# Optimization experiments

Measured on AMD Instinct MI355X. Metric: run time of the kernel, lower is better.

Reference implementation:

```python
import jax, jax.numpy as jnp
import numpy as np

B, N, D, H = 8, 577, 768, 12
HD = D // H
SCALE = HD ** -0.5
LN_EPS = 1e-5


def layer_norm(x, w, b):
    mu = jnp.mean(x, -1, keepdims=True)
    var = jnp.mean((x - mu) ** 2, -1, keepdims=True)
    return (x - mu) * jax.lax.rsqrt(var + LN_EPS) * w + b


def wasserstein_distance_matmul(mean1, cov1, mean2, cov2):
    # all [B,H,N,hd]; returns [B,H,N,N]
    m1_2 = jnp.sum(mean1 ** 2, -1, keepdims=True)
    m2_2 = jnp.sum(mean2 ** 2, -1, keepdims=True)
    ret = -2.0 * jnp.einsum('bhnd,bhmd->bhnm', mean1, mean2) + m1_2 + jnp.swapaxes(m2_2, -1, -2)
    c1s = jnp.sqrt(jnp.clip(cov1, 1e-24))
    c2s = jnp.sqrt(jnp.clip(cov2, 1e-24))
    cov_ret = (-2.0 * jnp.einsum('bhnd,bhmd->bhnm', c1s, c2s)
               + jnp.sum(cov1, -1, keepdims=True)
               + jnp.swapaxes(jnp.sum(cov2, -1, keepdims=True), -1, -2))
    return ret + cov_ret


def setup_inputs() -> dict:
    key = jax.random.key(0)
    ks = jax.random.split(key, 20)
    s = 0.02
    return {
        'x_mean': jax.random.normal(ks[0], (B, N, D), jnp.float32),
        'x_cov': jax.random.normal(ks[1], (B, N, D), jnp.float32),
        'rel_pos_bias': jax.random.normal(ks[2], (1, H, N, N), jnp.float32),
        'norm1_w': jnp.ones((D,), jnp.float32),
        'norm1_b': jnp.zeros((D,), jnp.float32),
        'qkv_w': jax.random.normal(ks[3], (3 * D, D), jnp.float32) * s,
        'proj_w': jax.random.normal(ks[4], (D, D), jnp.float32) * s,
        'proj_b': jnp.zeros((D,), jnp.float32),
        'cov_proj_w': jax.random.normal(ks[5], (D, D), jnp.float32) * s,
        'cov_proj_b': jnp.zeros((D,), jnp.float32),
        'norm2_w': jnp.ones((D,), jnp.float32),
        'norm2_b': jnp.zeros((D,), jnp.float32),
        'fc1_w': jax.random.normal(ks[6], (4 * D, D), jnp.float32) * s,
        'fc1_b': jnp.zeros((4 * D,), jnp.float32),
        'fc2_w': jax.random.normal(ks[7], (D, 4 * D), jnp.float32) * s,
        'fc2_b': jnp.zeros((D,), jnp.float32),
        'gamma1': 0.1 * jnp.ones((D,), jnp.float32),
        'gamma2': 0.1 * jnp.ones((D,), jnp.float32),
    }


def _split_heads(t):
    # [B,N,3D] -> q,k,v each [B,H,N,hd]
    t = t.reshape(B, N, 3, H, HD).transpose(2, 0, 3, 1, 4)
    return t[0], t[1], t[2]


def attention(xm, xc, rel_pos_bias, qkv_w, proj_w, proj_b, cov_proj_w, cov_proj_b):
    qkv = xm @ qkv_w.T                                  # [B,N,3D]
    q, k, v = _split_heads(qkv)
    cov_qkv = jax.nn.elu(xc @ qkv_w.T) + 1.0            # same weights for cov stream
    cov_q, cov_k, cov_v = _split_heads(cov_qkv)
    q = q * SCALE
    attn = -wasserstein_distance_matmul(q, cov_q, k, cov_k)
    attn = jax.nn.sigmoid(attn + 1e-24)
    attn = jax.nn.softmax(attn + rel_pos_bias, axis=-1)  # [B,H,N,N]
    mean_ctx = jnp.einsum('bhnm,bhmd->bhnd', attn, v).transpose(0, 2, 1, 3).reshape(B, N, D)
    cov_ctx = jnp.einsum('bhnm,bhmd->bhnd', attn ** 2, cov_v).transpose(0, 2, 1, 3).reshape(B, N, D)
    mean_out = mean_ctx @ proj_w.T + proj_b
    cov_out = cov_ctx @ cov_proj_w.T + cov_proj_b
    return mean_out, cov_out


def mlp(x, fc1_w, fc1_b, fc2_w, fc2_b):
    h = jax.nn.gelu(x @ fc1_w.T + fc1_b, approximate=False)
    return h @ fc2_w.T + fc2_b


def reference(x_mean, x_cov, rel_pos_bias, norm1_w, norm1_b, qkv_w, proj_w, proj_b,
              cov_proj_w, cov_proj_b, norm2_w, norm2_b, fc1_w, fc1_b, fc2_w, fc2_b,
              gamma1, gamma2):
    mean, cov = attention(layer_norm(x_mean, norm1_w, norm1_b),
                          layer_norm(x_cov, norm1_w, norm1_b),
                          rel_pos_bias, qkv_w, proj_w, proj_b, cov_proj_w, cov_proj_b)
    x_mean = x_mean + gamma1 * mean
    fcm = gamma2 * mlp(layer_norm(x_mean, norm2_w, norm2_b), fc1_w, fc1_b, fc2_w, fc2_b)
    x_cov = x_cov + gamma1 * cov
    fcc = gamma2 * mlp(layer_norm(x_cov, norm2_w, norm2_b), fc1_w, fc1_b, fc2_w, fc2_b)
    return (x_mean + fcm, x_cov + fcc)
```

## Files before the change

### kernel.cpp

```cpp
#include <hip/hip_runtime.h>
#include <hip/hip_bf16.h>
#include <math.h>
#include <stdint.h>

typedef __bf16 bf16;
typedef __attribute__((ext_vector_type(8))) __bf16 bf16x8;
typedef __attribute__((ext_vector_type(4))) float f32x4;

typedef __attribute__((address_space(1))) void gas_void;
typedef __attribute__((address_space(3))) void las_void;

#define DEV __device__ __forceinline__

static constexpr int B_ = 8, N_ = 577, D_ = 768, H_ = 12;
static constexpr int M_ = B_ * N_;
static constexpr int MP_ = 4736;
static constexpr int NP_ = 640;
static constexpr int BH_ = B_ * H_;
static constexpr float SCALE_ = 0.125f;

DEV void async_cp16(const void* g, void* l) {
  __builtin_amdgcn_global_load_lds((gas_void*)g, (las_void*)l, 16, 0, 0);
}
DEV float fast_rcp(float x) { return __builtin_amdgcn_rcpf(x); }
DEV float elu1(float x) { return x > 0.0f ? x + 1.0f : __expf(x); }
DEV float fast_gelu(float x) {
  const float x2 = x * x;
  const float z = x * fmaf(0.0713548826f, x2, 1.5957691216f);
  return x * fast_rcp(1.0f + __expf(-z));
}

__global__ __launch_bounds__(256) void cvt_kernel(const float* __restrict__ src,
                                                  bf16* __restrict__ dst, int n4) {
  const int i = blockIdx.x * 256 + threadIdx.x;
  if (i < n4) {
    const float4 v = ((const float4*)src)[i];
    bf16 o[4] = {(bf16)v.x, (bf16)v.y, (bf16)v.z, (bf16)v.w};
    *(uint64_t*)(dst + (size_t)i * 4) = *(const uint64_t*)o;
  }
}

__global__ __launch_bounds__(256) void ln_kernel(const float* __restrict__ x,
                                                 const float* __restrict__ w,
                                                 const float* __restrict__ bp,
                                                 bf16* __restrict__ out) {
  const int row = blockIdx.x;
  const int t = threadIdx.x;
  const float* xr = x + (size_t)row * D_;
  float v0 = xr[t], v1 = xr[t + 256], v2 = xr[t + 512];
  float s = v0 + v1 + v2;
  float ss = v0 * v0 + v1 * v1 + v2 * v2;
#pragma unroll
  for (int m = 32; m >= 1; m >>= 1) {
    s += __shfl_down(s, m);
    ss += __shfl_down(ss, m);
  }
  __shared__ float red[8];
  if ((t & 63) == 0) { red[t >> 6] = s; red[4 + (t >> 6)] = ss; }
  __syncthreads();
  s = red[0] + red[1] + red[2] + red[3];
  ss = red[4] + red[5] + red[6] + red[7];
  const float mu = s * (1.0f / D_);
  float var = ss * (1.0f / D_) - mu * mu;
  var = fmaxf(var, 0.0f);
  const float rs = rsqrtf(var + 1e-5f);
  bf16* orow = out + (size_t)row * D_;
  orow[t]       = (bf16)((v0 - mu) * rs * w[t]       + bp[t]);
  orow[t + 256] = (bf16)((v1 - mu) * rs * w[t + 256] + bp[t + 256]);
  orow[t + 512] = (bf16)((v2 - mu) * rs * w[t + 512] + bp[t + 512]);
}

enum { EP_BF16 = 0, EP_PROJ = 1, EP_GELU = 2, EP_FC2 = 3 };

template <int EP, int K>
__global__ __launch_bounds__(256) void gemm_bt(
    const bf16* __restrict__ A, const bf16* __restrict__ W0,
    const bf16* __restrict__ W1, int Nn, int gx,
    const float* __restrict__ bias0, const float* __restrict__ bias1,
    const float* __restrict__ gamma,
    const float* __restrict__ resid0, const float* __restrict__ resid1,
    bf16* __restrict__ Cb, float* __restrict__ Cf0, float* __restrict__ Cf1) {
  __shared__ __align__(16) bf16 As[3][128 * 32];
  __shared__ __align__(16) bf16 Bs[3][128 * 32];
  const int nwg = gridDim.x;
  const int o = blockIdx.x;
  const int q = nwg >> 3, r = nwg & 7, xcd = o & 7;
  const int flat = (xcd < r ? xcd * (q + 1) : r * (q + 1) + (xcd - r) * q) + (o >> 3);
  const int bx = flat % gx, by = flat / gx;

  const int t = threadIdx.x;
  const int lane = t & 63, wv = t >> 6;
  const int ln = lane & 15, kg = lane >> 4;
  const int wr = wv >> 1, wc = wv & 1;
  const int s = (int)(by >= (MP_ / 128));
  const bf16* W = s ? W1 : W0;
  const size_t brow = (size_t)by * 128;
  const size_t bcol = (size_t)bx * 128;
  const int r0 = t >> 2, gsl = t & 3;
  const bf16* A0 = A + (brow + r0) * (size_t)K + gsl * 8;
  const bf16* A1 = A + (brow + r0 + 64) * (size_t)K + gsl * 8;
  const bf16* W0p = W + (bcol + r0) * (size_t)K + gsl * 8;
  const bf16* W1p = W + (bcol + r0 + 64) * (size_t)K + gsl * 8;

  auto stage = [&](int buf, int kk) {
    async_cp16(A0 + kk, &As[buf][(wv * 64) * 8]);
    async_cp16(A1 + kk, &As[buf][(256 + wv * 64) * 8]);
    async_cp16(W0p + kk, &Bs[buf][(wv * 64) * 8]);
    async_cp16(W1p + kk, &Bs[buf][(256 + wv * 64) * 8]);
  };

  f32x4 acc[4][4] = {};
  constexpr int nt = K >> 5;
  static_assert(nt % 3 == 0, "K/32 must be divisible by 3");
  stage(0, 0);
  stage(1, 32);
#pragma unroll 1
  for (int tb = 0; tb < nt; tb += 3) {
#pragma unroll
    for (int u = 0; u < 3; u++) {
      const int tt = tb + u;
      if (tt + 1 < nt) {
        asm volatile("s_waitcnt vmcnt(4)" ::: "memory");
      } else {
        asm volatile("s_waitcnt vmcnt(0)" ::: "memory");
      }
      __builtin_amdgcn_s_barrier();
      bf16x8 af[4], bfr[4];
#pragma unroll
      for (int i = 0; i < 4; i++)
        af[i] = *(const bf16x8*)&As[u][(wr * 64 + i * 16 + ln) * 32 + kg * 8];
#pragma unroll
      for (int j = 0; j < 4; j++)
        bfr[j] = *(const bf16x8*)&Bs[u][(wc * 64 + j * 16 + ln) * 32 + kg * 8];
#pragma unroll
      for (int i = 0; i < 4; i++)
#pragma unroll
        for (int j = 0; j < 4; j++)
          acc[i][j] = __builtin_amdgcn_mfma_f32_16x16x32_bf16(af[i], bfr[j], acc[i][j], 0, 0, 0);
      if (tt + 2 < nt) stage((u + 2) % 3, (tt + 2) * 32);
    }
  }

  const float* biasS = s ? bias1 : bias0;
  const float* residS = s ? resid1 : resid0;
  float* CfS = s ? Cf1 : Cf0;
#pragma unroll
  for (int i = 0; i < 4; i++) {
    const int rb = (int)brow + wr * 64 + i * 16 + kg * 4;
#pragma unroll
    for (int j = 0; j < 4; j++) {
      const int col = (int)bcol + wc * 64 + j * 16 + ln;
#pragma unroll
      for (int rr = 0; rr < 4; rr++) {
        const int row = rb + rr;
        float v = acc[i][j][rr];
        if (EP == EP_BF16) {
          Cb[(size_t)row * Nn + col] = (bf16)v;
        } else if (EP == EP_GELU) {
          v += biasS[col];
          Cb[(size_t)row * Nn + col] = (bf16)fast_gelu(v);
        } else {
          const int r2 = row - s * MP_;
          if (r2 < M_) {
            v += biasS[col];
            if (EP == EP_PROJ) {
              CfS[(size_t)r2 * Nn + col] = residS[(size_t)r2 * Nn + col] + gamma[col] * v;
            } else {
              CfS[(size_t)r2 * Nn + col] += gamma[col] * v;
            }
          }
        }
      }
    }
  }
}

__global__ __launch_bounds__(256) void prep_kernel(
    const bf16* __restrict__ qm, const bf16* __restrict__ qc,
    bf16* __restrict__ Qcat, bf16* __restrict__ Kcat,
    bf16* __restrict__ Vt, bf16* __restrict__ CVt,
    float* __restrict__ rowt, float* __restrict__ colt) {
  const int n0 = blockIdx.x * 64;
  const int h = blockIdx.y, b = blockIdx.z;
  const int bh = b * H_ + h;
  const int t = threadIdx.x;
  const int nl = t >> 2, c = t & 3;
  const int n = n0 + nl;
  const bool valid = n < N_;
  __shared__ bf16 vts[64][72], cvts[64][72];
  float q2 = 0.f, cqs = 0.f, k2 = 0.f, cks = 0.f;
  bf16 qo[16], sqo[16], ko[16], sko[16];
  if (valid) {
    const size_t ro = (size_t)(b * N_ + n) * 2304 + h * 64 + c * 16;
#pragma unroll
    for (int half = 0; half < 2; half++) {
      bf16x8 qv8 = *(const bf16x8*)(qm + ro + half * 8);
      bf16x8 kv8 = *(const bf16x8*)(qm + ro + 768 + half * 8);
      bf16x8 vv8 = *(const bf16x8*)(qm + ro + 1536 + half * 8);
      bf16x8 cq8 = *(const bf16x8*)(qc + ro + half * 8);
      bf16x8 ck8 = *(const bf16x8*)(qc + ro + 768 + half * 8);
      bf16x8 cv8 = *(const bf16x8*)(qc + ro + 1536 + half * 8);
#pragma unroll
      for (int i = 0; i < 8; i++) {
        const int d = half * 8 + i;
        float qv = (float)qv8[i] * SCALE_;
        float kv = (float)kv8[i];
        float cq1 = elu1((float)cq8[i]);
        float ck1 = elu1((float)ck8[i]);
        q2 += qv * qv; cqs += cq1; k2 += kv * kv; cks += ck1;
        qo[d] = (bf16)qv; sqo[d] = (bf16)sqrtf(fmaxf(cq1, 1e-24f));
        ko[d] = (bf16)kv; sko[d] = (bf16)sqrtf(fmaxf(ck1, 1e-24f));
        vts[nl][c * 16 + d] = vv8[i];
        cvts[nl][c * 16 + d] = (bf16)elu1((float)cv8[i]);
      }
    }
  } else {
#pragma unroll
    for (int d = 0; d < 16; d++) {
      qo[d] = (bf16)0.f; sqo[d] = (bf16)0.f; ko[d] = (bf16)0.f; sko[d] = (bf16)0.f;
      vts[nl][c * 16 + d] = (bf16)0.f; cvts[nl][c * 16 + d] = (bf16)0.f;
    }
  }
  {
    bf16* qrow = Qcat + ((size_t)bh * NP_ + n) * 128;
    bf16* krow = Kcat + ((size_t)bh * NP_ + n) * 128;
#pragma unroll
    for (int d = 0; d < 16; d++) {
      qrow[c * 16 + d] = qo[d];
      qrow[64 + c * 16 + d] = sqo[d];
      krow[c * 16 + d] = ko[d];
      krow[64 + c * 16 + d] = sko[d];
    }
  }
  float rt = q2 + cqs, ct = k2 + cks;
  rt += __shfl_xor(rt, 1); rt += __shfl_xor(rt, 2);
  ct += __shfl_xor(ct, 1); ct += __shfl_xor(ct, 2);
  if (c == 0) { rowt[(size_t)bh * NP_ + n] = rt; colt[(size_t)bh * NP_ + n] = ct; }
  __syncthreads();
  const int drow = t >> 2;
  const size_t vb = ((size_t)bh * 64 + drow) * NP_ + n0 + c * 16;
#pragma unroll
  for (int i = 0; i < 16; i++) {
    Vt[vb + i] = vts[c * 16 + i][drow];
    CVt[vb + i] = cvts[c * 16 + i][drow];
  }
}

__global__ __launch_bounds__(256) void attn_kernel(
    const bf16* __restrict__ Qcat, const bf16* __restrict__ Kcat,
    const bf16* __restrict__ Vt, const bf16* __restrict__ CVt,
    const float* __restrict__ rowt, const float* __restrict__ colt,
    const bf16* __restrict__ bias,
    bf16* __restrict__ ctxm, bf16* __restrict__ ctxc) {
  const int id = blockIdx.x;
  const int xcd = id & 7, slot = id >> 3;
  const int g = xcd + 8 * (slot / 10);
  const int it = slot % 10;
  const int b = g / H_, h = g % H_;
  const int bh = g;
  const int i0 = it * 64;
  const int t = threadIdx.x;
  const int lane = t & 63, w = t >> 6;
  const int ln = lane & 15, kg = lane >> 4;
  __shared__ __align__(16) bf16 Ks[64 * 128];
  __shared__ __align__(16) bf16 Vs[64 * 64];
  __shared__ __align__(16) bf16 CVs[64 * 64];
  __shared__ __align__(16) bf16 Ps[64 * 72];

  const bf16* Qg = Qcat + (size_t)bh * NP_ * 128;
  const bf16* Kg = Kcat + (size_t)bh * NP_ * 128;
  const bf16* Vg = Vt + (size_t)bh * 64 * NP_;
  const bf16* CVg = CVt + (size_t)bh * 64 * NP_;

#pragma unroll
  for (int qq = 0; qq < 4; qq++) {
    const int idx = qq * 256 + t;
    const int row = idx >> 4, sl = idx & 15;
    async_cp16(Qg + (size_t)(i0 + row) * 128 + ((sl ^ (row & 7)) * 8),
               &Ks[(qq * 256 + w * 64) * 8]);
  }
  __syncthreads();
  bf16x8 aq[4];
  {
    const int row = w * 16 + ln;
#pragma unroll
    for (int kc = 0; kc < 4; kc++) {
      const int slot2 = kc * 4 + kg;
      aq[kc] = *(const bf16x8*)&Ks[row * 128 + ((slot2 ^ (row & 7)) * 8)];
    }
  }
  float rt[4];
#pragma unroll
  for (int r = 0; r < 4; r++) rt[r] = rowt[(size_t)bh * NP_ + i0 + w * 16 + kg * 4 + r];

  f32x4 accm[4] = {}, accc[4] = {};
  float den[4] = {0.f, 0.f, 0.f, 0.f};
  const int igb = i0 + w * 16 + kg * 4;

  for (int jt = 0; jt < 10; jt++) {
    const int j0 = jt * 64;
    __syncthreads();
#pragma unroll
    for (int qq = 0; qq < 4; qq++) {
      const int idx = qq * 256 + t;
      const int row = idx >> 4, sl = idx & 15;
      async_cp16(Kg + (size_t)(j0 + row) * 128 + ((sl ^ (row & 7)) * 8),
                 &Ks[(qq * 256 + w * 64) * 8]);
    }
#pragma unroll
    for (int qq = 0; qq < 2; qq++) {
      const int idx = qq * 256 + t;
      const int row = idx >> 3, sl = idx & 7;
      async_cp16(Vg + (size_t)row * NP_ + j0 + ((sl ^ (row & 7)) * 8),
                 &Vs[(qq * 256 + w * 64) * 8]);
      async_cp16(CVg + (size_t)row * NP_ + j0 + ((sl ^ (row & 7)) * 8),
                 &CVs[(qq * 256 + w * 64) * 8]);
    }
    float bb[4][4], ctb[4];
#pragma unroll
    for (int js = 0; js < 4; js++) {
      const int jg = j0 + js * 16 + ln;
      const int jc = jg < N_ ? jg : N_ - 1;
      ctb[js] = colt[(size_t)bh * NP_ + jg];
#pragma unroll
      for (int r = 0; r < 4; r++) {
        const int ic = (igb + r) < N_ ? (igb + r) : N_ - 1;
        bb[js][r] = (float)bias[((size_t)h * N_ + ic) * N_ + jc];
      }
    }
    __syncthreads();
#pragma unroll
    for (int js = 0; js < 4; js++) {
      f32x4 sv = {};
#pragma unroll
      for (int kc = 0; kc < 4; kc++) {
        const int row = js * 16 + ln;
        const int slot2 = kc * 4 + kg;
        bf16x8 bk = *(const bf16x8*)&Ks[row * 128 + ((slot2 ^ (row & 7)) * 8)];
        sv = __builtin_amdgcn_mfma_f32_16x16x32_bf16(aq[kc], bk, sv, 0, 0, 0);
      }
      const int jg = j0 + js * 16 + ln;
#pragma unroll
      for (int r = 0; r < 4; r++) {
        const float S = 2.0f * sv[r] - rt[r] - ctb[js];
        const float sig = fast_rcp(1.0f + __expf(-S));
        float e = __expf(sig + bb[js][r]);
        if (jg >= N_) e = 0.0f;
        const bf16 eb = (bf16)e;
        den[r] += (float)eb;
        Ps[(w * 16 + kg * 4 + r) * 72 + js * 16 + ln] = eb;
      }
    }
#pragma unroll
    for (int ks = 0; ks < 2; ks++) {
      const int prow = w * 16 + ln;
      bf16x8 pa = *(const bf16x8*)&Ps[prow * 72 + ks * 32 + kg * 8];
      bf16x8 p2a;
#pragma unroll
      for (int i = 0; i < 8; i++) {
        const float pf = (float)pa[i];
        p2a[i] = (bf16)(pf * pf);
      }
#pragma unroll
      for (int nt = 0; nt < 4; nt++) {
        const int vrow = nt * 16 + ln;
        const int slot2 = ks * 4 + kg;
        bf16x8 vb = *(const bf16x8*)&Vs[vrow * 64 + ((slot2 ^ (vrow & 7)) * 8)];
        bf16x8 cvb = *(const bf16x8*)&CVs[vrow * 64 + ((slot2 ^ (vrow & 7)) * 8)];
        accm[nt] = __builtin_amdgcn_mfma_f32_16x16x32_bf16(pa, vb, accm[nt], 0, 0, 0);
        accc[nt] = __builtin_amdgcn_mfma_f32_16x16x32_bf16(p2a, cvb, accc[nt], 0, 0, 0);
      }
    }
  }
#pragma unroll
  for (int r = 0; r < 4; r++) {
    float d = den[r];
    d += __shfl_xor(d, 1); d += __shfl_xor(d, 2);
    d += __shfl_xor(d, 4); d += __shfl_xor(d, 8);
    den[r] = d;
  }
#pragma unroll
  for (int r = 0; r < 4; r++) {
    const int ig = i0 + w * 16 + kg * 4 + r;
    if (ig < N_) {
      const float inv = fast_rcp(den[r]);
      const float inv2 = inv * inv;
      const size_t base = (size_t)(b * N_ + ig) * D_ + h * 64;
#pragma unroll
      for (int nt = 0; nt < 4; nt++) {
        ctxm[base + nt * 16 + ln] = (bf16)(accm[nt][r] * inv);
        ctxc[base + nt * 16 + ln] = (bf16)(accc[nt][r] * inv2);
      }
    }
  }
}

extern "C" void kernel_launch(void* const* d_in, const int* in_sizes, int n_in,
                              void* d_out, int out_size, void* d_ws, size_t ws_size,
                              hipStream_t stream) {
  const float* x_mean = (const float*)d_in[0];
  const float* x_cov  = (const float*)d_in[1];
  const float* rpb    = (const float*)d_in[2];
  const float* n1w    = (const float*)d_in[3];
  const float* n1b    = (const float*)d_in[4];
  const float* qkvw   = (const float*)d_in[5];
  const float* projw  = (const float*)d_in[6];
  const float* projb  = (const float*)d_in[7];
  const float* cprojw = (const float*)d_in[8];
  const float* cprojb = (const float*)d_in[9];
  const float* n2w    = (const float*)d_in[10];
  const float* n2b    = (const float*)d_in[11];
  const float* fc1w   = (const float*)d_in[12];
  const float* fc1b   = (const float*)d_in[13];
  const float* fc2w   = (const float*)d_in[14];
  const float* fc2b   = (const float*)d_in[15];
  const float* g1     = (const float*)d_in[16];
  const float* g2     = (const float*)d_in[17];
  (void)in_sizes; (void)n_in; (void)out_size; (void)ws_size;

  char* ws = (char*)d_ws;
  size_t off = 0;
  auto take = [&](size_t bytes) {
    char* p = ws + off;
    off += (bytes + 255) & ~(size_t)255;
    return p;
  };
  bf16* wq   = (bf16*)take((size_t)2304 * 768 * 2);
  bf16* wp   = (bf16*)take((size_t)768 * 768 * 2);
  bf16* wcp  = (bf16*)take((size_t)768 * 768 * 2);
  bf16* wf1  = (bf16*)take((size_t)3072 * 768 * 2);
  bf16* wf2  = (bf16*)take((size_t)768 * 3072 * 2);
  bf16* xln  = (bf16*)take((size_t)2 * MP_ * 768 * 2);
  char* R    = take((size_t)2 * MP_ * 3072 * 2);
  bf16* qkvb = (bf16*)R;
  bf16* hbuf = (bf16*)R;
  bf16* biasb = (bf16*)(R + (size_t)2 * MP_ * 2304 * 2);
  bf16* Qcat = (bf16*)take((size_t)BH_ * NP_ * 128 * 2);
  bf16* Kcat = (bf16*)take((size_t)BH_ * NP_ * 128 * 2);
  bf16* Vt   = (bf16*)take((size_t)BH_ * 64 * NP_ * 2);
  bf16* CVt  = (bf16*)take((size_t)BH_ * 64 * NP_ * 2);
  float* rowt = (float*)take((size_t)BH_ * NP_ * 4);
  float* colt = (float*)take((size_t)BH_ * NP_ * 4);
  bf16* ctx  = (bf16*)take((size_t)2 * MP_ * 768 * 2);

  float* outm = (float*)d_out;
  float* outc = outm + (size_t)M_ * D_;

  cvt_kernel<<<(2304 * 768 / 4 + 255) / 256, 256, 0, stream>>>(qkvw, wq, 2304 * 768 / 4);
  cvt_kernel<<<(768 * 768 / 4 + 255) / 256, 256, 0, stream>>>(projw, wp, 768 * 768 / 4);
  cvt_kernel<<<(768 * 768 / 4 + 255) / 256, 256, 0, stream>>>(cprojw, wcp, 768 * 768 / 4);
  cvt_kernel<<<(3072 * 768 / 4 + 255) / 256, 256, 0, stream>>>(fc1w, wf1, 3072 * 768 / 4);
  cvt_kernel<<<(768 * 3072 / 4 + 255) / 256, 256, 0, stream>>>(fc2w, wf2, 768 * 3072 / 4);
  cvt_kernel<<<(H_ * N_ * N_ / 4 + 255) / 256, 256, 0, stream>>>(rpb, biasb, H_ * N_ * N_ / 4);
  ln_kernel<<<M_, 256, 0, stream>>>(x_mean, n1w, n1b, xln);
  ln_kernel<<<M_, 256, 0, stream>>>(x_cov, n1w, n1b, xln + (size_t)MP_ * 768);
  gemm_bt<EP_BF16, 768><<<18 * 74, 256, 0, stream>>>(xln, wq, wq, 2304, 18,
      nullptr, nullptr, nullptr, nullptr, nullptr, qkvb, nullptr, nullptr);
  prep_kernel<<<dim3(10, 12, 8), 256, 0, stream>>>(
      qkvb, qkvb + (size_t)MP_ * 2304, Qcat, Kcat, Vt, CVt, rowt, colt);
  attn_kernel<<<960, 256, 0, stream>>>(Qcat, Kcat, Vt, CVt, rowt, colt, biasb,
                                       ctx, ctx + (size_t)MP_ * 768);
  gemm_bt<EP_PROJ, 768><<<6 * 74, 256, 0, stream>>>(ctx, wp, wcp, 768, 6,
      projb, cprojb, g1, x_mean, x_cov, nullptr, outm, outc);
  ln_kernel<<<M_, 256, 0, stream>>>(outm, n2w, n2b, xln);
  ln_kernel<<<M_, 256, 0, stream>>>(outc, n2w, n2b, xln + (size_t)MP_ * 768);
  gemm_bt<EP_GELU, 768><<<24 * 74, 256, 0, stream>>>(xln, wf1, wf1, 3072, 24,
      fc1b, fc1b, nullptr, nullptr, nullptr, hbuf, nullptr, nullptr);
  gemm_bt<EP_FC2, 3072><<<6 * 74, 256, 0, stream>>>(hbuf, wf2, wf2, 768, 6,
      fc2b, fc2b, g2, nullptr, nullptr, nullptr, outm, outc);
}
```

Measured before the change: 385.7 us.

## Enlarge GEMM tiles to 256x128 with 8 waves and earlier prefetch issue

The GEMM kernel moves from a 128x128 tile with 4 waves to a 256x128 tile with 8 waves (512 threads), so each staged weight tile is reused across twice as many rows. A rows are clamped and stores are masked so tiles can straddle the padded boundary between the mean and cov halves. The prefetch of the next stage is also issued right after the barrier instead of after the MFMAs, for better overlap of loads with compute. The risks are fewer workgroups, which hurts wave fill for the smaller proj and fc2 GEMMs, plus wasted work in the padded rows of the last tile.

```diff
diff --git a/kernel.cpp b/kernel.cpp
--- a/kernel.cpp
+++ b/kernel.cpp
@@ -73,40 +73,45 @@
 enum { EP_BF16 = 0, EP_PROJ = 1, EP_GELU = 2, EP_FC2 = 3 };
 
 template <int EP, int K>
-__global__ __launch_bounds__(256) void gemm_bt(
-    const bf16* __restrict__ A, const bf16* __restrict__ W0,
-    const bf16* __restrict__ W1, int Nn, int gx,
+__global__ __launch_bounds__(512, 4) void gemm_bt(
+    const bf16* __restrict__ A0, const bf16* __restrict__ A1,
+    const bf16* __restrict__ W0, const bf16* __restrict__ W1,
+    int Nn, int gx,
     const float* __restrict__ bias0, const float* __restrict__ bias1,
     const float* __restrict__ gamma,
     const float* __restrict__ resid0, const float* __restrict__ resid1,
     bf16* __restrict__ Cb, float* __restrict__ Cf0, float* __restrict__ Cf1) {
-  __shared__ __align__(16) bf16 As[3][128 * 32];
-  __shared__ __align__(16) bf16 Bs[3][128 * 32];
+  __shared__ __align__(16) bf16 As[3 * 8192];
+  __shared__ __align__(16) bf16 Bs[3 * 4096];
   const int nwg = gridDim.x;
   const int o = blockIdx.x;
   const int q = nwg >> 3, r = nwg & 7, xcd = o & 7;
   const int flat = (xcd < r ? xcd * (q + 1) : r * (q + 1) + (xcd - r) * q) + (o >> 3);
   const int bx = flat % gx, by = flat / gx;
 
+  const int s = (int)(by >= 19);
+  const int byl = by - (s ? 19 : 0);
+  const bf16* A = s ? A1 : A0;
+  const bf16* W = s ? W1 : W0;
+  const int brow = byl * 256;
+  const int bcol = bx * 128;
+
   const int t = threadIdx.x;
   const int lane = t & 63, wv = t >> 6;
   const int ln = lane & 15, kg = lane >> 4;
   const int wr = wv >> 1, wc = wv & 1;
-  const int s = (int)(by >= (MP_ / 128));
-  const bf16* W = s ? W1 : W0;
-  const size_t brow = (size_t)by * 128;
-  const size_t bcol = (size_t)bx * 128;
+
   const int r0 = t >> 2, gsl = t & 3;
-  const bf16* A0 = A + (brow + r0) * (size_t)K + gsl * 8;
-  const bf16* A1 = A + (brow + r0 + 64) * (size_t)K + gsl * 8;
-  const bf16* W0p = W + (bcol + r0) * (size_t)K + gsl * 8;
-  const bf16* W1p = W + (bcol + r0 + 64) * (size_t)K + gsl * 8;
+  const int ra0 = min(brow + r0, MP_ - 1);
+  const int ra1 = min(brow + 128 + r0, MP_ - 1);
+  const bf16* Asrc0 = A + (size_t)ra0 * K + gsl * 8;
+  const bf16* Asrc1 = A + (size_t)ra1 * K + gsl * 8;
+  const bf16* Bsrc  = W + (size_t)(bcol + r0) * K + gsl * 8;
 
   auto stage = [&](int buf, int kk) {
-    async_cp16(A0 + kk, &As[buf][(wv * 64) * 8]);
-    async_cp16(A1 + kk, &As[buf][(256 + wv * 64) * 8]);
-    async_cp16(W0p + kk, &Bs[buf][(wv * 64) * 8]);
-    async_cp16(W1p + kk, &Bs[buf][(256 + wv * 64) * 8]);
+    async_cp16(Asrc0 + kk, &As[buf * 8192 + wv * 512]);
+    async_cp16(Asrc1 + kk, &As[buf * 8192 + 4096 + wv * 512]);
+    async_cp16(Bsrc + kk,  &Bs[buf * 4096 + wv * 512]);
   };
 
   f32x4 acc[4][4] = {};
@@ -114,30 +119,33 @@
   static_assert(nt % 3 == 0, "K/32 must be divisible by 3");
   stage(0, 0);
   stage(1, 32);
+  const int aoff = (wr * 64 + ln) * 32 + kg * 8;
+  const int boff = (wc * 64 + ln) * 32 + kg * 8;
 #pragma unroll 1
   for (int tb = 0; tb < nt; tb += 3) {
 #pragma unroll
     for (int u = 0; u < 3; u++) {
       const int tt = tb + u;
       if (tt + 1 < nt) {
-        asm volatile("s_waitcnt vmcnt(4)" ::: "memory");
+        asm volatile("s_waitcnt vmcnt(3)" ::: "memory");
       } else {
         asm volatile("s_waitcnt vmcnt(0)" ::: "memory");
       }
       __builtin_amdgcn_s_barrier();
+      asm volatile("" ::: "memory");
+      if (tt + 2 < nt) stage((u + 2) % 3, (tt + 2) * 32);
       bf16x8 af[4], bfr[4];
 #pragma unroll
       for (int i = 0; i < 4; i++)
-        af[i] = *(const bf16x8*)&As[u][(wr * 64 + i * 16 + ln) * 32 + kg * 8];
+        af[i] = *(const bf16x8*)&As[u * 8192 + aoff + i * 512];
 #pragma unroll
       for (int j = 0; j < 4; j++)
-        bfr[j] = *(const bf16x8*)&Bs[u][(wc * 64 + j * 16 + ln) * 32 + kg * 8];
+        bfr[j] = *(const bf16x8*)&Bs[u * 4096 + boff + j * 512];
 #pragma unroll
       for (int i = 0; i < 4; i++)
 #pragma unroll
         for (int j = 0; j < 4; j++)
           acc[i][j] = __builtin_amdgcn_mfma_f32_16x16x32_bf16(af[i], bfr[j], acc[i][j], 0, 0, 0);
-      if (tt + 2 < nt) stage((u + 2) % 3, (tt + 2) * 32);
     }
   }
 
@@ -146,28 +154,30 @@
   float* CfS = s ? Cf1 : Cf0;
 #pragma unroll
   for (int i = 0; i < 4; i++) {
-    const int rb = (int)brow + wr * 64 + i * 16 + kg * 4;
+    const int rb = brow + wr * 64 + i * 16 + kg * 4;
 #pragma unroll
     for (int j = 0; j < 4; j++) {
-      const int col = (int)bcol + wc * 64 + j * 16 + ln;
+      const int col = bcol + wc * 64 + j * 16 + ln;
 #pragma unroll
       for (int rr = 0; rr < 4; rr++) {
-        const int row = rb + rr;
+        const int rowl = rb + rr;
         float v = acc[i][j][rr];
         if (EP == EP_BF16) {
-          Cb[(size_t)row * Nn + col] = (bf16)v;
+          if (rowl < MP_) Cb[((size_t)(s * MP_ + rowl)) * Nn + col] = (bf16)v;
         } else if (EP == EP_GELU) {
-          v += biasS[col];
-          Cb[(size_t)row * Nn + col] = (bf16)fast_gelu(v);
+          if (rowl < MP_) {
+            v += biasS[col];
+            Cb[((size_t)(s * MP_ + rowl)) * Nn + col] = (bf16)fast_gelu(v);
+          }
+        } else if (EP == EP_PROJ) {
+          if (rowl < M_) {
+            v += biasS[col];
+            CfS[(size_t)rowl * Nn + col] = residS[(size_t)rowl * Nn + col] + gamma[col] * v;
+          }
         } else {
-          const int r2 = row - s * MP_;
-          if (r2 < M_) {
+          if (rowl < M_) {
             v += biasS[col];
-            if (EP == EP_PROJ) {
-              CfS[(size_t)r2 * Nn + col] = residS[(size_t)r2 * Nn + col] + gamma[col] * v;
-            } else {
-              CfS[(size_t)r2 * Nn + col] += gamma[col] * v;
-            }
+            CfS[(size_t)rowl * Nn + col] += gamma[col] * v;
           }
         }
       }
@@ -454,18 +464,22 @@
   cvt_kernel<<<(H_ * N_ * N_ / 4 + 255) / 256, 256, 0, stream>>>(rpb, biasb, H_ * N_ * N_ / 4);
   ln_kernel<<<M_, 256, 0, stream>>>(x_mean, n1w, n1b, xln);
   ln_kernel<<<M_, 256, 0, stream>>>(x_cov, n1w, n1b, xln + (size_t)MP_ * 768);
-  gemm_bt<EP_BF16, 768><<<18 * 74, 256, 0, stream>>>(xln, wq, wq, 2304, 18,
+  gemm_bt<EP_BF16, 768><<<18 * 38, 512, 0, stream>>>(
+      xln, xln + (size_t)MP_ * 768, wq, wq, 2304, 18,
       nullptr, nullptr, nullptr, nullptr, nullptr, qkvb, nullptr, nullptr);
   prep_kernel<<<dim3(10, 12, 8), 256, 0, stream>>>(
       qkvb, qkvb + (size_t)MP_ * 2304, Qcat, Kcat, Vt, CVt, rowt, colt);
   attn_kernel<<<960, 256, 0, stream>>>(Qcat, Kcat, Vt, CVt, rowt, colt, biasb,
                                        ctx, ctx + (size_t)MP_ * 768);
-  gemm_bt<EP_PROJ, 768><<<6 * 74, 256, 0, stream>>>(ctx, wp, wcp, 768, 6,
+  gemm_bt<EP_PROJ, 768><<<6 * 38, 512, 0, stream>>>(
+      ctx, ctx + (size_t)MP_ * 768, wp, wcp, 768, 6,
       projb, cprojb, g1, x_mean, x_cov, nullptr, outm, outc);
   ln_kernel<<<M_, 256, 0, stream>>>(outm, n2w, n2b, xln);
   ln_kernel<<<M_, 256, 0, stream>>>(outc, n2w, n2b, xln + (size_t)MP_ * 768);
-  gemm_bt<EP_GELU, 768><<<24 * 74, 256, 0, stream>>>(xln, wf1, wf1, 3072, 24,
+  gemm_bt<EP_GELU, 768><<<24 * 38, 512, 0, stream>>>(
+      xln, xln + (size_t)MP_ * 768, wf1, wf1, 3072, 24,
       fc1b, fc1b, nullptr, nullptr, nullptr, hbuf, nullptr, nullptr);
-  gemm_bt<EP_FC2, 3072><<<6 * 74, 256, 0, stream>>>(hbuf, wf2, wf2, 768, 6,
+  gemm_bt<EP_FC2, 3072><<<6 * 38, 512, 0, stream>>>(
+      hbuf, hbuf + (size_t)MP_ * 3072, wf2, wf2, 768, 6,
       fc2b, fc2b, g2, nullptr, nullptr, nullptr, outm, outc);
 }
```

Measured after the change: 403.0 us. 4.5% more time.

## Add 256x256-tile 8-wave GEMM for QKV and FC1 projections

Applied to the files above, without the earlier changes.

Introduces a new GEMM kernel with 256x256 output tiles, 512 threads and 64-wide K steps. It uses double-buffered async global-to-LDS copies with XOR-swizzled LDS layout, staggered prefetch interleaved with MFMA phases, and setprio around the MFMA bursts. The QKV and FC1 GEMMs switch to it to raise arithmetic intensity and cut LDS/global traffic per flop. The larger tile wastes more work on the padded M edge, uses 128KB of LDS, and gives fewer workgroups per GEMM, which may hurt occupancy or load balance.

```diff
diff --git a/kernel.cpp b/kernel.cpp
--- a/kernel.cpp
+++ b/kernel.cpp
@@ -72,8 +72,174 @@
 
 enum { EP_BF16 = 0, EP_PROJ = 1, EP_GELU = 2, EP_FC2 = 3 };
 
+#define MFMA16(Q)                                                                        \
+  __builtin_amdgcn_s_setprio(1);                                                         \
+  _Pragma("unroll") for (int n = 0; n < 4; ++n) {                                        \
+    acc[2*(Q)][n]   = __builtin_amdgcn_mfma_f32_16x16x32_bf16(a0, bfr[n][0], acc[2*(Q)][n], 0, 0, 0);   \
+    acc[2*(Q)][n]   = __builtin_amdgcn_mfma_f32_16x16x32_bf16(a1, bfr[n][1], acc[2*(Q)][n], 0, 0, 0);   \
+    acc[2*(Q)+1][n] = __builtin_amdgcn_mfma_f32_16x16x32_bf16(a2, bfr[n][0], acc[2*(Q)+1][n], 0, 0, 0); \
+    acc[2*(Q)+1][n] = __builtin_amdgcn_mfma_f32_16x16x32_bf16(a3, bfr[n][1], acc[2*(Q)+1][n], 0, 0, 0); \
+  }                                                                                      \
+  __builtin_amdgcn_s_setprio(0);
+
+#define LDA4(Q)                                                   \
+  bf16x8 a0, a1, a2, a3;                                          \
+  {                                                               \
+    const int rA0_ = bb + (arow + (2*(Q)) * 16) * 64;             \
+    const int rA1_ = bb + (arow + (2*(Q)+1) * 16) * 64;           \
+    a0 = *(const bf16x8*)&As[rA0_ + sw0];                         \
+    a1 = *(const bf16x8*)&As[rA0_ + sw1];                         \
+    a2 = *(const bf16x8*)&As[rA1_ + sw0];                         \
+    a3 = *(const bf16x8*)&As[rA1_ + sw1];                         \
+  }
+
+#define SYNC_PRE()                    \
+  __builtin_amdgcn_sched_barrier(0);  \
+  __builtin_amdgcn_s_barrier();       \
+  __builtin_amdgcn_sched_barrier(0);
+
+#define SYNC_POST()                   \
+  __builtin_amdgcn_sched_barrier(0);  \
+  __builtin_amdgcn_s_barrier();       \
+  __builtin_amdgcn_sched_barrier(0);
+
 template <int EP, int K>
-__global__ __launch_bounds__(256) void gemm_bt(
+__global__ __launch_bounds__(512, 2) void gemm_big(
+    const bf16* __restrict__ A0s, const bf16* __restrict__ A1s,
+    const bf16* __restrict__ W0, const bf16* __restrict__ W1,
+    int Nn, int gx, const float* __restrict__ bias,
+    bf16* __restrict__ Cb) {
+  __shared__ __align__(16) bf16 As[2 * 16384];
+  __shared__ __align__(16) bf16 Bs[2 * 16384];
+  const int nwg = gridDim.x, o = blockIdx.x;
+  const int qd = nwg >> 3, rm = nwg & 7, xcd = o & 7;
+  const int flat = (xcd < rm ? xcd * (qd + 1) : rm * (qd + 1) + (xcd - rm) * qd) + (o >> 3);
+  const int bx = flat % gx, by = flat / gx;
+  const int s = (int)(by >= 19);
+  const int brow = (by - (s ? 19 : 0)) * 256;
+  const int bcol = bx * 256;
+  const bf16* A = s ? A1s : A0s;
+  const bf16* W = s ? W1 : W0;
+
+  const int t = threadIdx.x;
+  const int w = t >> 6, l = t & 63;
+  const int ln = l & 15, kg = l >> 4;
+  const int wr = w >> 2, wc = w & 3;
+
+  const int lr = l >> 3;
+  const int lcol = ((l & 7) ^ lr) * 8;
+  const int rb0 = w * 8 + lr;
+  const int rb1 = 64 + w * 8 + lr;
+  int rA;
+  rA = brow + rb0;       rA = rA < MP_ ? rA : MP_ - 1;
+  const bf16* sA00 = A + (size_t)rA * K + lcol;
+  rA = brow + rb1;       rA = rA < MP_ ? rA : MP_ - 1;
+  const bf16* sA01 = A + (size_t)rA * K + lcol;
+  rA = brow + 128 + rb0; rA = rA < MP_ ? rA : MP_ - 1;
+  const bf16* sA10 = A + (size_t)rA * K + lcol;
+  rA = brow + 128 + rb1; rA = rA < MP_ ? rA : MP_ - 1;
+  const bf16* sA11 = A + (size_t)rA * K + lcol;
+  const bf16* sB00 = W + (size_t)(bcol + rb0) * K + lcol;
+  const bf16* sB01 = W + (size_t)(bcol + rb1) * K + lcol;
+  const bf16* sB10 = W + (size_t)(bcol + 128 + rb0) * K + lcol;
+  const bf16* sB11 = W + (size_t)(bcol + 128 + rb1) * K + lcol;
+
+  auto st2 = [&](bf16* lds0, const bf16* g0, const bf16* g1, int kk) {
+    async_cp16(g0 + kk, lds0);
+    async_cp16(g1 + kk, lds0 + 4096);
+  };
+
+  const int arow = wr * 128 + ln;
+  const int bcolr = wc * 64 + ln;
+  const int sw0 = ((0 + kg) ^ (ln & 7)) * 8;
+  const int sw1 = ((4 + kg) ^ (ln & 7)) * 8;
+
+  f32x4 acc[8][4] = {};
+  bf16x8 bfr[4][2];
+  constexpr int nkt = K / 64;
+  static_assert(K % 64 == 0, "K multiple of 64");
+
+  st2(&As[w * 512], sA00, sA01, 0);
+  st2(&As[8192 + w * 512], sA10, sA11, 0);
+  st2(&Bs[w * 512], sB00, sB01, 0);
+  st2(&Bs[8192 + w * 512], sB10, sB11, 0);
+  st2(&Bs[16384 + w * 512], sB00, sB01, 64);
+  st2(&Bs[16384 + 8192 + w * 512], sB10, sB11, 64);
+  __builtin_amdgcn_sched_barrier(0);
+  asm volatile("s_waitcnt vmcnt(4)" ::: "memory");
+  __builtin_amdgcn_s_barrier();
+  __builtin_amdgcn_sched_barrier(0);
+
+#pragma unroll 1
+  for (int tt = 0; tt < nkt; ++tt) {
+    const int bb = (tt & 1) * 16384;
+    const int bn = bb ^ 16384;
+    const int kk1 = (tt + 1) * 64, kk2 = (tt + 2) * 64;
+    const bool s1 = (tt + 1) < nkt, s2 = (tt + 2) < nkt;
+    {
+      LDA4(0)
+#pragma unroll
+      for (int n = 0; n < 4; ++n) {
+        const int cb = bb + (bcolr + n * 16) * 64;
+        bfr[n][0] = *(const bf16x8*)&Bs[cb + sw0];
+        bfr[n][1] = *(const bf16x8*)&Bs[cb + sw1];
+      }
+      if (s1) st2(&As[bn + w * 512], sA00, sA01, kk1);
+      SYNC_PRE()
+      MFMA16(0)
+      SYNC_POST()
+    }
+    {
+      LDA4(1)
+      if (s1) st2(&As[bn + 8192 + w * 512], sA10, sA11, kk1);
+      SYNC_PRE()
+      MFMA16(1)
+      SYNC_POST()
+    }
+    {
+      LDA4(2)
+      if (s2) st2(&Bs[bb + w * 512], sB00, sB01, kk2);
+      SYNC_PRE()
+      MFMA16(2)
+      SYNC_POST()
+    }
+    {
+      LDA4(3)
+      if (s2) st2(&Bs[bb + 8192 + w * 512], sB10, sB11, kk2);
+      __builtin_amdgcn_sched_barrier(0);
+      if (s2) {
+        asm volatile("s_waitcnt vmcnt(4)" ::: "memory");
+      } else if (s1) {
+        asm volatile("s_waitcnt vmcnt(0)" ::: "memory");
+      }
+      __builtin_amdgcn_s_barrier();
+      __builtin_amdgcn_sched_barrier(0);
+      MFMA16(3)
+      SYNC_POST()
+    }
+  }
+
+#pragma unroll
+  for (int m = 0; m < 8; ++m) {
+    const int rbse = brow + wr * 128 + m * 16 + kg * 4;
+#pragma unroll
+    for (int n = 0; n < 4; ++n) {
+      const int col = bcol + wc * 64 + n * 16 + ln;
+#pragma unroll
+      for (int e = 0; e < 4; ++e) {
+        const int rl = rbse + e;
+        if (rl < MP_) {
+          float v = acc[m][n][e];
+          if (EP == EP_GELU) { v += bias[col]; v = fast_gelu(v); }
+          Cb[((size_t)(s * MP_ + rl)) * Nn + col] = (bf16)v;
+        }
+      }
+    }
+  }
+}
+
+template <int EP, int K>
+__global__ __launch_bounds__(256) void gemm_sm(
     const bf16* __restrict__ A, const bf16* __restrict__ W0,
     const bf16* __restrict__ W1, int Nn, int gx,
     const float* __restrict__ bias0, const float* __restrict__ bias1,
@@ -454,18 +620,18 @@
   cvt_kernel<<<(H_ * N_ * N_ / 4 + 255) / 256, 256, 0, stream>>>(rpb, biasb, H_ * N_ * N_ / 4);
   ln_kernel<<<M_, 256, 0, stream>>>(x_mean, n1w, n1b, xln);
   ln_kernel<<<M_, 256, 0, stream>>>(x_cov, n1w, n1b, xln + (size_t)MP_ * 768);
-  gemm_bt<EP_BF16, 768><<<18 * 74, 256, 0, stream>>>(xln, wq, wq, 2304, 18,
-      nullptr, nullptr, nullptr, nullptr, nullptr, qkvb, nullptr, nullptr);
+  gemm_big<EP_BF16, 768><<<9 * 38, 512, 0, stream>>>(
+      xln, xln + (size_t)MP_ * 768, wq, wq, 2304, 9, nullptr, qkvb);
   prep_kernel<<<dim3(10, 12, 8), 256, 0, stream>>>(
       qkvb, qkvb + (size_t)MP_ * 2304, Qcat, Kcat, Vt, CVt, rowt, colt);
   attn_kernel<<<960, 256, 0, stream>>>(Qcat, Kcat, Vt, CVt, rowt, colt, biasb,
                                        ctx, ctx + (size_t)MP_ * 768);
-  gemm_bt<EP_PROJ, 768><<<6 * 74, 256, 0, stream>>>(ctx, wp, wcp, 768, 6,
+  gemm_sm<EP_PROJ, 768><<<6 * 74, 256, 0, stream>>>(ctx, wp, wcp, 768, 6,
       projb, cprojb, g1, x_mean, x_cov, nullptr, outm, outc);
   ln_kernel<<<M_, 256, 0, stream>>>(outm, n2w, n2b, xln);
   ln_kernel<<<M_, 256, 0, stream>>>(outc, n2w, n2b, xln + (size_t)MP_ * 768);
-  gemm_bt<EP_GELU, 768><<<24 * 74, 256, 0, stream>>>(xln, wf1, wf1, 3072, 24,
-      fc1b, fc1b, nullptr, nullptr, nullptr, hbuf, nullptr, nullptr);
-  gemm_bt<EP_FC2, 3072><<<6 * 74, 256, 0, stream>>>(hbuf, wf2, wf2, 768, 6,
+  gemm_big<EP_GELU, 768><<<12 * 38, 512, 0, stream>>>(
+      xln, xln + (size_t)MP_ * 768, wf1, wf1, 3072, 12, fc1b, hbuf);
+  gemm_sm<EP_FC2, 3072><<<6 * 74, 256, 0, stream>>>(hbuf, wf2, wf2, 768, 6,
       fc2b, fc2b, g2, nullptr, nullptr, nullptr, outm, outc);
 }
```

Result: slower. 412.2 us (+6.9%).

## Double-buffer K tiles in attention, load V directly to registers, merge small launches

Applied to the files above, without the earlier changes.

The attention kernel now double-buffers the K tile in shared memory, prefetching the next tile while the current one is computed. It also loads V and CV fragments straight from global memory into registers instead of staging them through LDS, which leaves one barrier per iteration instead of two. Separately, the six weight/bias conversion launches are merged into one segmented kernel, and each pair of LayerNorm launches into one. The trade-off is more register pressure from holding V fragments and uncoalesced direct global reads of V, in exchange for less launch overhead and fewer synchronisations.

```diff
diff --git a/kernel.cpp b/kernel.cpp
--- a/kernel.cpp
+++ b/kernel.cpp
@@ -30,23 +30,41 @@
   return x * fast_rcp(1.0f + __expf(-z));
 }
 
-__global__ __launch_bounds__(256) void cvt_kernel(const float* __restrict__ src,
-                                                  bf16* __restrict__ dst, int n4) {
-  const int i = blockIdx.x * 256 + threadIdx.x;
-  if (i < n4) {
-    const float4 v = ((const float4*)src)[i];
+__global__ __launch_bounds__(256) void cvt6_kernel(
+    const float* __restrict__ s0, const float* __restrict__ s1,
+    const float* __restrict__ s2, const float* __restrict__ s3,
+    const float* __restrict__ s4, const float* __restrict__ s5,
+    bf16* __restrict__ d0, bf16* __restrict__ d1, bf16* __restrict__ d2,
+    bf16* __restrict__ d3, bf16* __restrict__ d4, bf16* __restrict__ d5,
+    int n0, int n1, int n2, int n3, int n4c, int n5) {
+  const float* ss[6] = {s0, s1, s2, s3, s4, s5};
+  bf16* dd[6] = {d0, d1, d2, d3, d4, d5};
+  const int nn[6] = {n0, n1, n2, n3, n4c, n5};
+  int bid = blockIdx.x;
+  int seg = 0;
+#pragma unroll 6
+  for (int k = 0; k < 6; k++) {
+    const int nb = (nn[k] + 255) >> 8;
+    if (bid < nb) { seg = k; break; }
+    bid -= nb;
+  }
+  const int i = bid * 256 + threadIdx.x;
+  if (i < nn[seg]) {
+    const float4 v = ((const float4*)ss[seg])[i];
     bf16 o[4] = {(bf16)v.x, (bf16)v.y, (bf16)v.z, (bf16)v.w};
-    *(uint64_t*)(dst + (size_t)i * 4) = *(const uint64_t*)o;
-  }
-}
-
-__global__ __launch_bounds__(256) void ln_kernel(const float* __restrict__ x,
-                                                 const float* __restrict__ w,
-                                                 const float* __restrict__ bp,
-                                                 bf16* __restrict__ out) {
+    *(uint64_t*)(dd[seg] + (size_t)i * 4) = *(const uint64_t*)o;
+  }
+}
+
+__global__ __launch_bounds__(256) void ln2_kernel(
+    const float* __restrict__ x0, const float* __restrict__ x1,
+    const float* __restrict__ w, const float* __restrict__ bp,
+    bf16* __restrict__ out) {
   const int row = blockIdx.x;
+  const int st = (int)(row >= M_);
+  const int srow = row - st * M_;
+  const float* xr = (st ? x1 : x0) + (size_t)srow * D_;
   const int t = threadIdx.x;
-  const float* xr = x + (size_t)row * D_;
   float v0 = xr[t], v1 = xr[t + 256], v2 = xr[t + 512];
   float s = v0 + v1 + v2;
   float ss = v0 * v0 + v1 * v1 + v2 * v2;
@@ -64,7 +82,7 @@
   float var = ss * (1.0f / D_) - mu * mu;
   var = fmaxf(var, 0.0f);
   const float rs = rsqrtf(var + 1e-5f);
-  bf16* orow = out + (size_t)row * D_;
+  bf16* orow = out + ((size_t)st * MP_ + srow) * D_;
   orow[t]       = (bf16)((v0 - mu) * rs * w[t]       + bp[t]);
   orow[t + 256] = (bf16)((v1 - mu) * rs * w[t + 256] + bp[t + 256]);
   orow[t + 512] = (bf16)((v2 - mu) * rs * w[t + 512] + bp[t + 512]);
@@ -262,9 +280,7 @@
   const int t = threadIdx.x;
   const int lane = t & 63, w = t >> 6;
   const int ln = lane & 15, kg = lane >> 4;
-  __shared__ __align__(16) bf16 Ks[64 * 128];
-  __shared__ __align__(16) bf16 Vs[64 * 64];
-  __shared__ __align__(16) bf16 CVs[64 * 64];
+  __shared__ __align__(16) bf16 Ks[2][64 * 128];
   __shared__ __align__(16) bf16 Ps[64 * 72];
 
   const bf16* Qg = Qcat + (size_t)bh * NP_ * 128;
@@ -277,7 +293,14 @@
     const int idx = qq * 256 + t;
     const int row = idx >> 4, sl = idx & 15;
     async_cp16(Qg + (size_t)(i0 + row) * 128 + ((sl ^ (row & 7)) * 8),
-               &Ks[(qq * 256 + w * 64) * 8]);
+               &Ks[0][(qq * 256 + w * 64) * 8]);
+  }
+#pragma unroll
+  for (int qq = 0; qq < 4; qq++) {
+    const int idx = qq * 256 + t;
+    const int row = idx >> 4, sl = idx & 15;
+    async_cp16(Kg + (size_t)row * 128 + ((sl ^ (row & 7)) * 8),
+               &Ks[1][(qq * 256 + w * 64) * 8]);
   }
   __syncthreads();
   bf16x8 aq[4];
@@ -286,12 +309,13 @@
 #pragma unroll
     for (int kc = 0; kc < 4; kc++) {
       const int slot2 = kc * 4 + kg;
-      aq[kc] = *(const bf16x8*)&Ks[row * 128 + ((slot2 ^ (row & 7)) * 8)];
+      aq[kc] = *(const bf16x8*)&Ks[0][row * 128 + ((slot2 ^ (row & 7)) * 8)];
     }
   }
   float rt[4];
 #pragma unroll
   for (int r = 0; r < 4; r++) rt[r] = rowt[(size_t)bh * NP_ + i0 + w * 16 + kg * 4 + r];
+  __syncthreads();
 
   f32x4 accm[4] = {}, accc[4] = {};
   float den[4] = {0.f, 0.f, 0.f, 0.f};
@@ -299,23 +323,26 @@
 
   for (int jt = 0; jt < 10; jt++) {
     const int j0 = jt * 64;
-    __syncthreads();
-#pragma unroll
-    for (int qq = 0; qq < 4; qq++) {
-      const int idx = qq * 256 + t;
-      const int row = idx >> 4, sl = idx & 15;
-      async_cp16(Kg + (size_t)(j0 + row) * 128 + ((sl ^ (row & 7)) * 8),
-                 &Ks[(qq * 256 + w * 64) * 8]);
-    }
-#pragma unroll
-    for (int qq = 0; qq < 2; qq++) {
-      const int idx = qq * 256 + t;
-      const int row = idx >> 3, sl = idx & 7;
-      async_cp16(Vg + (size_t)row * NP_ + j0 + ((sl ^ (row & 7)) * 8),
-                 &Vs[(qq * 256 + w * 64) * 8]);
-      async_cp16(CVg + (size_t)row * NP_ + j0 + ((sl ^ (row & 7)) * 8),
-                 &CVs[(qq * 256 + w * 64) * 8]);
-    }
+    const int cur = 1 - (jt & 1), nxt = jt & 1;
+    if (jt + 1 < 10) {
+      const int jn = (jt + 1) * 64;
+#pragma unroll
+      for (int qq = 0; qq < 4; qq++) {
+        const int idx = qq * 256 + t;
+        const int row = idx >> 4, sl = idx & 15;
+        async_cp16(Kg + (size_t)(jn + row) * 128 + ((sl ^ (row & 7)) * 8),
+                   &Ks[nxt][(qq * 256 + w * 64) * 8]);
+      }
+    }
+    bf16x8 vfr[2][4], cvfr[2][4];
+#pragma unroll
+    for (int ks = 0; ks < 2; ks++)
+#pragma unroll
+      for (int nt = 0; nt < 4; nt++) {
+        const size_t a = (size_t)(nt * 16 + ln) * NP_ + j0 + ks * 32 + kg * 8;
+        vfr[ks][nt] = *(const bf16x8*)(Vg + a);
+        cvfr[ks][nt] = *(const bf16x8*)(CVg + a);
+      }
     float bb[4][4], ctb[4];
 #pragma unroll
     for (int js = 0; js < 4; js++) {
@@ -328,7 +355,6 @@
         bb[js][r] = (float)bias[((size_t)h * N_ + ic) * N_ + jc];
       }
     }
-    __syncthreads();
 #pragma unroll
     for (int js = 0; js < 4; js++) {
       f32x4 sv = {};
@@ -336,7 +362,7 @@
       for (int kc = 0; kc < 4; kc++) {
         const int row = js * 16 + ln;
         const int slot2 = kc * 4 + kg;
-        bf16x8 bk = *(const bf16x8*)&Ks[row * 128 + ((slot2 ^ (row & 7)) * 8)];
+        bf16x8 bk = *(const bf16x8*)&Ks[cur][row * 128 + ((slot2 ^ (row & 7)) * 8)];
         sv = __builtin_amdgcn_mfma_f32_16x16x32_bf16(aq[kc], bk, sv, 0, 0, 0);
       }
       const int jg = j0 + js * 16 + ln;
@@ -363,14 +389,11 @@
       }
 #pragma unroll
       for (int nt = 0; nt < 4; nt++) {
-        const int vrow = nt * 16 + ln;
-        const int slot2 = ks * 4 + kg;
-        bf16x8 vb = *(const bf16x8*)&Vs[vrow * 64 + ((slot2 ^ (vrow & 7)) * 8)];
-        bf16x8 cvb = *(const bf16x8*)&CVs[vrow * 64 + ((slot2 ^ (vrow & 7)) * 8)];
-        accm[nt] = __builtin_amdgcn_mfma_f32_16x16x32_bf16(pa, vb, accm[nt], 0, 0, 0);
-        accc[nt] = __builtin_amdgcn_mfma_f32_16x16x32_bf16(p2a, cvb, accc[nt], 0, 0, 0);
-      }
-    }
+        accm[nt] = __builtin_amdgcn_mfma_f32_16x16x32_bf16(pa, vfr[ks][nt], accm[nt], 0, 0, 0);
+        accc[nt] = __builtin_amdgcn_mfma_f32_16x16x32_bf16(p2a, cvfr[ks][nt], accc[nt], 0, 0, 0);
+      }
+    }
+    __syncthreads();
   }
 #pragma unroll
   for (int r = 0; r < 4; r++) {
@@ -446,14 +469,16 @@
   float* outm = (float*)d_out;
   float* outc = outm + (size_t)M_ * D_;
 
-  cvt_kernel<<<(2304 * 768 / 4 + 255) / 256, 256, 0, stream>>>(qkvw, wq, 2304 * 768 / 4);
-  cvt_kernel<<<(768 * 768 / 4 + 255) / 256, 256, 0, stream>>>(projw, wp, 768 * 768 / 4);
-  cvt_kernel<<<(768 * 768 / 4 + 255) / 256, 256, 0, stream>>>(cprojw, wcp, 768 * 768 / 4);
-  cvt_kernel<<<(3072 * 768 / 4 + 255) / 256, 256, 0, stream>>>(fc1w, wf1, 3072 * 768 / 4);
-  cvt_kernel<<<(768 * 3072 / 4 + 255) / 256, 256, 0, stream>>>(fc2w, wf2, 768 * 3072 / 4);
-  cvt_kernel<<<(H_ * N_ * N_ / 4 + 255) / 256, 256, 0, stream>>>(rpb, biasb, H_ * N_ * N_ / 4);
-  ln_kernel<<<M_, 256, 0, stream>>>(x_mean, n1w, n1b, xln);
-  ln_kernel<<<M_, 256, 0, stream>>>(x_cov, n1w, n1b, xln + (size_t)MP_ * 768);
+  {
+    const int c0 = 2304 * 768 / 4, c1 = 768 * 768 / 4, c2 = 768 * 768 / 4;
+    const int c3 = 3072 * 768 / 4, c4 = 768 * 3072 / 4, c5 = H_ * N_ * N_ / 4;
+    const int nb = ((c0 + 255) >> 8) + ((c1 + 255) >> 8) + ((c2 + 255) >> 8) +
+                   ((c3 + 255) >> 8) + ((c4 + 255) >> 8) + ((c5 + 255) >> 8);
+    cvt6_kernel<<<nb, 256, 0, stream>>>(qkvw, projw, cprojw, fc1w, fc2w, rpb,
+                                        wq, wp, wcp, wf1, wf2, biasb,
+                                        c0, c1, c2, c3, c4, c5);
+  }
+  ln2_kernel<<<2 * M_, 256, 0, stream>>>(x_mean, x_cov, n1w, n1b, xln);
   gemm_bt<EP_BF16, 768><<<18 * 74, 256, 0, stream>>>(xln, wq, wq, 2304, 18,
       nullptr, nullptr, nullptr, nullptr, nullptr, qkvb, nullptr, nullptr);
   prep_kernel<<<dim3(10, 12, 8), 256, 0, stream>>>(
@@ -462,8 +487,7 @@
                                        ctx, ctx + (size_t)MP_ * 768);
   gemm_bt<EP_PROJ, 768><<<6 * 74, 256, 0, stream>>>(ctx, wp, wcp, 768, 6,
       projb, cprojb, g1, x_mean, x_cov, nullptr, outm, outc);
-  ln_kernel<<<M_, 256, 0, stream>>>(outm, n2w, n2b, xln);
-  ln_kernel<<<M_, 256, 0, stream>>>(outc, n2w, n2b, xln + (size_t)MP_ * 768);
+  ln2_kernel<<<2 * M_, 256, 0, stream>>>(outm, outc, n2w, n2b, xln);
   gemm_bt<EP_GELU, 768><<<24 * 74, 256, 0, stream>>>(xln, wf1, wf1, 3072, 24,
       fc1b, fc1b, nullptr, nullptr, nullptr, hbuf, nullptr, nullptr);
   gemm_bt<EP_FC2, 3072><<<6 * 74, 256, 0, stream>>>(hbuf, wf2, wf2, 768, 6,
```

Measured after the change: 404.3 us. 4.8% more time.
